# Kernel tuning notes

Measured on AMD Instinct MI355X. Metric: run time of the kernel, lower is better.

The kernel has to match this reference:

```python
import jax, jax.numpy as jnp
import numpy as np

BETA = 0.001
VAR_MIN = 1e-7


def setup_inputs() -> dict:
    key = jax.random.key(0)
    ks = jax.random.split(key, 16)
    B, IN, N, Z, S = 2048, 32, 1024, 8, 8
    f32 = jnp.float32
    return {
        "batch": jax.random.normal(ks[0], (B, IN, N, 2), f32),
        "labels": jax.random.randint(ks[1], (B, 1), 0, 2).astype(jnp.int32),
        "eps1": jax.random.normal(ks[2], (B, S, Z), f32),
        "eps2": jax.random.normal(ks[3], (B, S, Z), f32),
        "W1": jax.random.normal(ks[4], (IN, 32), f32) / np.sqrt(IN),
        "b1": jax.random.normal(ks[5], (32,), f32) * 0.01,
        "W2": jax.random.normal(ks[6], (32, 32), f32) / np.sqrt(32),
        "b2": jax.random.normal(ks[7], (32,), f32) * 0.01,
        "Wmu": jax.random.normal(ks[8], (32, Z), f32) / np.sqrt(32),
        "bmu": jax.random.normal(ks[9], (Z,), f32) * 0.01,
        "Wv": jax.random.normal(ks[10], (32, Z), f32) / np.sqrt(32),
        "bv": jax.random.normal(ks[11], (Z,), f32) * 0.01,
        "sw": jax.random.normal(ks[12], (1, 1), f32),
        "sb": jax.random.normal(ks[13], (1,), f32),
    }


def _cal_z(data, W1, b1, W2, b2, Wmu, bmu, Wv, bv):
    # data: [B, IN, N] -> points [B, N, IN]
    x = jnp.transpose(data, (0, 2, 1))
    h = jax.nn.relu(x @ W1 + b1)
    h = jax.nn.relu(h @ W2 + b2)
    mu = h @ Wmu + bmu                    # [B, N, Z]
    var = jax.nn.softplus(h @ Wv + bv)    # [B, N, Z]
    var = jnp.maximum(var, VAR_MIN)
    var_pog = 1.0 / jnp.sum(1.0 / var, axis=1)  # [B, Z]
    # Faithful to torch source: var is reassigned before mu update, so
    # mu = var_pog * sum(mu / var_pog) == sum(mu) over the N axis.
    mu_pog = jnp.sum(mu, axis=1)                # [B, Z]
    return mu_pog, var_pog


def _kl(mu, var):
    # KL(N(mu, sqrt(var)) || N(0, 1)), elementwise, then mean
    return jnp.mean(-0.5 * jnp.log(var) + 0.5 * (var + mu * mu) - 0.5)


def reference(batch, labels, eps1, eps2, W1, b1, W2, b2, Wmu, bmu, Wv, bv, sw, sb):
    mu1, var1 = _cal_z(batch[:, :, :, 0], W1, b1, W2, b2, Wmu, bmu, Wv, bv)
    mu2, var2 = _cal_z(batch[:, :, :, 1], W1, b1, W2, b2, Wmu, bmu, Wv, bv)

    kl = (_kl(mu1, var1) + _kl(mu2, var2)) * BETA

    # rsample: mu + sigma * eps, [B, S, Z]
    z1 = mu1[:, None, :] + jnp.sqrt(var1)[:, None, :] * eps1
    z2 = mu2[:, None, :] + jnp.sqrt(var2)[:, None, :] * eps2

    # pairwise distances over the S x S sample grid: [B, S, S]
    diff = z1[:, :, None, :] - z2[:, None, :, :]
    dist = jnp.sqrt(jnp.sum(diff * diff, axis=-1))

    a = jax.nn.softplus(sw[0, 0])
    p = jax.nn.sigmoid(-a * dist + sb[0])
    loss1 = -jnp.log(p)
    loss_1 = jnp.mean(loss1, axis=(1, 2), keepdims=False)[:, None]  # [B, 1]
    # Faithful bug in torch source: loss0 is never assigned, stays zero,
    # so the (1 - labels) term contributes nothing.
    labels_f = labels.astype(loss_1.dtype)
    soft = jnp.mean(loss_1 * labels_f)

    return kl + soft
```

## Files before the change

### kernel.cpp

```cpp
#include <hip/hip_runtime.h>
#include <hip/hip_bf16.h>

#define B_   2048
#define N_   1024
#define BETA 0.001f
#define VAR_MIN 1e-7f

#define PTS   64
#define NSTG  (N_ / PTS)
#define RF    128

typedef __attribute__((ext_vector_type(8))) short  bf16x8;
typedef __attribute__((ext_vector_type(4))) float  f32x4;
typedef __attribute__((ext_vector_type(4))) unsigned int u32x4;

__device__ __forceinline__ unsigned short f2bf_u(float x) {
    __hip_bfloat16 h = __float2bfloat16(x);
    return __builtin_bit_cast(unsigned short, h);
}
__device__ __forceinline__ unsigned int cvtpk(float lo, float hi) {
    unsigned int r;
    asm("v_cvt_pk_bf16_f32 %0, %1, %2" : "=v"(r) : "v"(lo), "v"(hi));
    return r;
}
__device__ __forceinline__ float softplus_cheap(float x) {
    float sp = __logf(1.f + __expf(x));
    return x > 15.f ? x : sp;
}
__device__ __forceinline__ float rcp_fast(float x) {
    return __builtin_amdgcn_rcpf(x);
}
__device__ __forceinline__ float softplus_ref(float x) {
    return x > 20.f ? x : log1pf(expf(x));
}
__device__ __forceinline__ float iv_of(float x) {
    return rcp_fast(fmaxf(softplus_cheap(x), VAR_MIN));
}

__device__ __forceinline__ int kperm(int k) {
    return 4 * (k >> 3) + (k & 3) + 16 * ((k >> 2) & 1);
}

extern "C" __global__ void hib_prep(const float* __restrict__ W1,
                                    const float* __restrict__ W2,
                                    const float* __restrict__ Wmu,
                                    const float* __restrict__ Wv,
                                    unsigned short* __restrict__ wf)
{
    const int l = threadIdx.x;
    const int r = l & 15, kb = l >> 4;
    const int kbr = r >> 2, ri = r & 3;
#pragma unroll
    for (int j = 0; j < 8; j++) {
        const int k1 = kb * 8 + j;
        const int kp = kperm(k1);
        wf[(0 * 64 + l) * 8 + j] = f2bf_u(W1[k1 * 32 + r]);
        wf[(1 * 64 + l) * 8 + j] = f2bf_u(W1[k1 * 32 + 16 + r]);
        wf[(2 * 64 + l) * 8 + j] = f2bf_u(W2[kp * 32 + r]);
        wf[(3 * 64 + l) * 8 + j] = f2bf_u(W2[kp * 32 + 16 + r]);
        wf[(4 * 64 + l) * 8 + j] = f2bf_u(ri < 2 ? Wmu[kp * 8 + 2 * kbr + ri]
                                                 : Wv[kp * 8 + 2 * kbr + (ri - 2)]);
    }
}

__device__ __forceinline__ bf16x8 pack_relu(f32x4 a, f32x4 b) {
    u32x4 w;
    w[0] = cvtpk(fmaxf(a[0], 0.f), fmaxf(a[1], 0.f));
    w[1] = cvtpk(fmaxf(a[2], 0.f), fmaxf(a[3], 0.f));
    w[2] = cvtpk(fmaxf(b[0], 0.f), fmaxf(b[1], 0.f));
    w[3] = cvtpk(fmaxf(b[2], 0.f), fmaxf(b[3], 0.f));
    return __builtin_bit_cast(bf16x8, w);
}

__device__ __forceinline__ void red16(f32x4& v) {
#pragma unroll
    for (int off = 8; off; off >>= 1) {
        v[0] += __shfl_down(v[0], off);
        v[1] += __shfl_down(v[1], off);
        v[2] += __shfl_down(v[2], off);
        v[3] += __shfl_down(v[3], off);
    }
}

__device__ __forceinline__ void stage_issue(const float* __restrict__ bbase,
                                            float* __restrict__ ldsbuf,
                                            int st, int wid, int l)
{
    const int sub = l >> 5, lo = l & 31;
#pragma unroll
    for (int q = 0; q < 4; ++q) {
        const int row = wid * 8 + q * 2;
        const float* gs = bbase + (size_t)(row + sub) * (2 * N_) + st * RF + lo * 4;
        __builtin_amdgcn_global_load_lds(
            (const __attribute__((address_space(1))) unsigned int*)gs,
            (__attribute__((address_space(3))) unsigned int*)&ldsbuf[row * RF],
            16, 0, 0);
    }
}

__global__ void __launch_bounds__(256, 4)
hib_mfma(const float* __restrict__ batch,
         const int* __restrict__ labels,
         const float* __restrict__ eps1, const float* __restrict__ eps2,
         const unsigned short* __restrict__ wf,
         const float* __restrict__ b1, const float* __restrict__ b2,
         const float* __restrict__ bmu, const float* __restrict__ bv,
         const float* __restrict__ sw, const float* __restrict__ sb,
         float* __restrict__ out)
{
    __shared__ float lds[2][32 * RF];
    __shared__ float sacc[32];

    const int tid = threadIdx.x;
    const int b   = blockIdx.x;
    const int wid = tid >> 6, l = tid & 63;
    const int c   = l & 15, kb = l >> 4;

    if (tid < 32) sacc[tid] = 0.f;

    const bf16x8* wfv = (const bf16x8*)wf;
    const bf16x8 A1a = wfv[0 * 64 + l], A1b = wfv[1 * 64 + l];
    const bf16x8 A2a = wfv[2 * 64 + l], A2b = wfv[3 * 64 + l];
    const bf16x8 Ahd = wfv[4 * 64 + l];

    const int r4 = 4 * kb;
    const int z2 = 2 * kb;
    f32x4 c1a, c1b, c2a, c2b, chd;
    c1a[0] = b1[r4];      c1a[1] = b1[r4 + 1];      c1a[2] = b1[r4 + 2];      c1a[3] = b1[r4 + 3];
    c1b[0] = b1[16 + r4]; c1b[1] = b1[16 + r4 + 1]; c1b[2] = b1[16 + r4 + 2]; c1b[3] = b1[16 + r4 + 3];
    c2a[0] = b2[r4];      c2a[1] = b2[r4 + 1];      c2a[2] = b2[r4 + 2];      c2a[3] = b2[r4 + 3];
    c2b[0] = b2[16 + r4]; c2b[1] = b2[16 + r4 + 1]; c2b[2] = b2[16 + r4 + 2]; c2b[3] = b2[16 + r4 + 3];
    chd[0] = bmu[z2]; chd[1] = bmu[z2 + 1];
    chd[2] = bv[z2];  chd[3] = bv[z2 + 1];

    f32x4 acc0 = {0.f, 0.f, 0.f, 0.f};
    f32x4 acc1 = {0.f, 0.f, 0.f, 0.f};

    const float* bbase = batch + (size_t)b * 32 * (2 * N_);

    stage_issue(bbase, lds[0], 0, wid, l);
    __syncthreads();

    int buf = 0;
#pragma unroll 1
    for (int t = 0; t < NSTG; ++t) {
        if (t + 1 < NSTG)
            stage_issue(bbase, lds[buf ^ 1], t + 1, wid, l);

        float2 xr[8];
#pragma unroll
        for (int j = 0; j < 8; j++)
            xr[j] = *(const float2*)&lds[buf][(kb * 8 + j) * RF + (wid * 16 + c) * 2];

        u32x4 w0, w1;
        w0[0] = cvtpk(xr[0].x, xr[1].x); w0[1] = cvtpk(xr[2].x, xr[3].x);
        w0[2] = cvtpk(xr[4].x, xr[5].x); w0[3] = cvtpk(xr[6].x, xr[7].x);
        w1[0] = cvtpk(xr[0].y, xr[1].y); w1[1] = cvtpk(xr[2].y, xr[3].y);
        w1[2] = cvtpk(xr[4].y, xr[5].y); w1[3] = cvtpk(xr[6].y, xr[7].y);
        const bf16x8 f0 = __builtin_bit_cast(bf16x8, w0);
        const bf16x8 f1 = __builtin_bit_cast(bf16x8, w1);

        f32x4 d1a0 = __builtin_amdgcn_mfma_f32_16x16x32_bf16(A1a, f0, c1a, 0, 0, 0);
        f32x4 d1b0 = __builtin_amdgcn_mfma_f32_16x16x32_bf16(A1b, f0, c1b, 0, 0, 0);
        f32x4 d1a1 = __builtin_amdgcn_mfma_f32_16x16x32_bf16(A1a, f1, c1a, 0, 0, 0);
        f32x4 d1b1 = __builtin_amdgcn_mfma_f32_16x16x32_bf16(A1b, f1, c1b, 0, 0, 0);

        bf16x8 p20 = pack_relu(d1a0, d1b0);
        bf16x8 p21 = pack_relu(d1a1, d1b1);

        f32x4 d2a0 = __builtin_amdgcn_mfma_f32_16x16x32_bf16(A2a, p20, c2a, 0, 0, 0);
        f32x4 d2b0 = __builtin_amdgcn_mfma_f32_16x16x32_bf16(A2b, p20, c2b, 0, 0, 0);
        f32x4 d2a1 = __builtin_amdgcn_mfma_f32_16x16x32_bf16(A2a, p21, c2a, 0, 0, 0);
        f32x4 d2b1 = __builtin_amdgcn_mfma_f32_16x16x32_bf16(A2b, p21, c2b, 0, 0, 0);

        bf16x8 p30 = pack_relu(d2a0, d2b0);
        bf16x8 p31 = pack_relu(d2a1, d2b1);

        f32x4 e0 = __builtin_amdgcn_mfma_f32_16x16x32_bf16(Ahd, p30, chd, 0, 0, 0);
        f32x4 e1 = __builtin_amdgcn_mfma_f32_16x16x32_bf16(Ahd, p31, chd, 0, 0, 0);

        acc0[0] += e0[0];        acc0[1] += e0[1];
        acc0[2] += iv_of(e0[2]); acc0[3] += iv_of(e0[3]);
        acc1[0] += e1[0];        acc1[1] += e1[1];
        acc1[2] += iv_of(e1[2]); acc1[3] += iv_of(e1[3]);

        __syncthreads();
        buf ^= 1;
    }

    red16(acc0);
    red16(acc1);

    if (c == 0) {
        atomicAdd(&sacc[z2],          acc0[0]);
        atomicAdd(&sacc[z2 + 1],      acc0[1]);
        atomicAdd(&sacc[16 + z2],     acc0[2]);
        atomicAdd(&sacc[16 + z2 + 1], acc0[3]);
        atomicAdd(&sacc[8 + z2],      acc1[0]);
        atomicAdd(&sacc[8 + z2 + 1],  acc1[1]);
        atomicAdd(&sacc[24 + z2],     acc1[2]);
        atomicAdd(&sacc[24 + z2 + 1], acc1[3]);
    }
    __syncthreads();

    if (tid < 64) {
        const float a    = softplus_ref(sw[0]);
        const float sbv_ = sb[0];

        float muA[8], muB[8], sgA[8], sgB[8];
#pragma unroll
        for (int z = 0; z < 8; z++) {
            muA[z] = sacc[z];
            muB[z] = sacc[8 + z];
            sgA[z] = sqrtf(1.0f / sacc[16 + z]);
            sgB[z] = sqrtf(1.0f / sacc[24 + z]);
        }
        const int i = tid >> 3, j = tid & 7;
        float d2 = 0.f;
#pragma unroll
        for (int z = 0; z < 8; z++) {
            float e1 = eps1[((size_t)b * 8 + i) * 8 + z];
            float e2 = eps2[((size_t)b * 8 + j) * 8 + z];
            float zz1 = fmaf(sgA[z], e1, muA[z]);
            float zz2 = fmaf(sgB[z], e2, muB[z]);
            float d = zz1 - zz2;
            d2 = fmaf(d, d, d2);
        }
        const float lab = (float)labels[b];
        float contrib = softplus_ref(a * sqrtf(d2) - sbv_) * lab
                      * (1.0f / (64.0f * (float)B_));

        if (tid < 16) {
            const int cc = tid >> 3, z = tid & 7;
            float iv  = sacc[16 + cc * 8 + z];
            float var = 1.0f / iv;
            float m   = sacc[cc * 8 + z];
            contrib += (-0.5f * logf(var) + 0.5f * (var + m * m) - 0.5f)
                       * (BETA / (8.0f * (float)B_));
        }
#pragma unroll
        for (int off = 32; off; off >>= 1) contrib += __shfl_down(contrib, off);
        if (tid == 0) atomicAdd(out, contrib);
    }
}

extern "C" void kernel_launch(void* const* d_in, const int* in_sizes, int n_in,
                              void* d_out, int out_size, void* d_ws, size_t ws_size,
                              hipStream_t stream)
{
    (void)in_sizes; (void)n_in; (void)out_size; (void)ws_size;
    const float* batch  = (const float*)d_in[0];
    const int*   labels = (const int*)  d_in[1];
    const float* eps1   = (const float*)d_in[2];
    const float* eps2   = (const float*)d_in[3];
    const float* W1     = (const float*)d_in[4];
    const float* b1     = (const float*)d_in[5];
    const float* W2     = (const float*)d_in[6];
    const float* b2     = (const float*)d_in[7];
    const float* Wmu    = (const float*)d_in[8];
    const float* bmu    = (const float*)d_in[9];
    const float* Wv     = (const float*)d_in[10];
    const float* bv     = (const float*)d_in[11];
    const float* sw     = (const float*)d_in[12];
    const float* sb     = (const float*)d_in[13];

    unsigned short* wf = (unsigned short*)d_ws;

    hipMemsetAsync(d_out, 0, sizeof(float), stream);
    hib_prep<<<1, 64, 0, stream>>>(W1, W2, Wmu, Wv, wf);
    hib_mfma<<<B_, 256, 0, stream>>>(batch, labels, eps1, eps2, wf,
                                     b1, b2, bmu, bv, sw, sb, (float*)d_out);
}
```

Before: 128.1 us.

## Give each wave a private double-buffered LDS slice and drop block barriers

```diff
diff --git a/kernel.cpp b/kernel.cpp
--- a/kernel.cpp
+++ b/kernel.cpp
@@ -6,9 +6,7 @@
 #define BETA 0.001f
 #define VAR_MIN 1e-7f
 
-#define PTS   64
-#define NSTG  (N_ / PTS)
-#define RF    128
+#define NIT  16
 
 typedef __attribute__((ext_vector_type(8))) short  bf16x8;
 typedef __attribute__((ext_vector_type(4))) float  f32x4;
@@ -82,18 +80,19 @@
     }
 }
 
-__device__ __forceinline__ void stage_issue(const float* __restrict__ bbase,
-                                            float* __restrict__ ldsbuf,
-                                            int st, int wid, int l)
-{
-    const int sub = l >> 5, lo = l & 31;
+__device__ __forceinline__ void stage_wp(const float* __restrict__ bbase,
+                                         float* __restrict__ buf,
+                                         int it, int wid, int l)
+{
+    const int lrow = l >> 3, lcol = (l & 7) * 4;
+    const int colbase = (wid * 256 + it * 16) * 2;
 #pragma unroll
     for (int q = 0; q < 4; ++q) {
-        const int row = wid * 8 + q * 2;
-        const float* gs = bbase + (size_t)(row + sub) * (2 * N_) + st * RF + lo * 4;
+        const int row = q * 8 + lrow;
+        const float* gs = bbase + (size_t)row * (2 * N_) + colbase + lcol;
         __builtin_amdgcn_global_load_lds(
             (const __attribute__((address_space(1))) unsigned int*)gs,
-            (__attribute__((address_space(3))) unsigned int*)&ldsbuf[row * RF],
+            (__attribute__((address_space(3))) unsigned int*)&buf[q * 8 * 32],
             16, 0, 0);
     }
 }
@@ -108,7 +107,7 @@
          const float* __restrict__ sw, const float* __restrict__ sb,
          float* __restrict__ out)
 {
-    __shared__ float lds[2][32 * RF];
+    __shared__ float lds[4][2][32 * 32];
     __shared__ float sacc[32];
 
     const int tid = threadIdx.x;
@@ -137,20 +136,21 @@
     f32x4 acc1 = {0.f, 0.f, 0.f, 0.f};
 
     const float* bbase = batch + (size_t)b * 32 * (2 * N_);
-
-    stage_issue(bbase, lds[0], 0, wid, l);
+    float* bufA = &lds[wid][0][0];
+    float* bufB = &lds[wid][1][0];
+
+    stage_wp(bbase, bufA, 0, wid, l);
+    stage_wp(bbase, bufB, 1, wid, l);
     __syncthreads();
 
-    int buf = 0;
 #pragma unroll 1
-    for (int t = 0; t < NSTG; ++t) {
-        if (t + 1 < NSTG)
-            stage_issue(bbase, lds[buf ^ 1], t + 1, wid, l);
+    for (int it = 0; it < NIT; ++it) {
+        float* cur = (it & 1) ? bufB : bufA;
 
         float2 xr[8];
 #pragma unroll
         for (int j = 0; j < 8; j++)
-            xr[j] = *(const float2*)&lds[buf][(kb * 8 + j) * RF + (wid * 16 + c) * 2];
+            xr[j] = *(const float2*)&cur[(kb * 8 + j) * 32 + c * 2];
 
         u32x4 w0, w1;
         w0[0] = cvtpk(xr[0].x, xr[1].x); w0[1] = cvtpk(xr[2].x, xr[3].x);
@@ -160,6 +160,12 @@
         const bf16x8 f0 = __builtin_bit_cast(bf16x8, w0);
         const bf16x8 f1 = __builtin_bit_cast(bf16x8, w1);
 
+        asm volatile("s_waitcnt lgkmcnt(0)" ::: "memory");
+        __builtin_amdgcn_sched_barrier(0);
+        if (it + 2 < NIT)
+            stage_wp(bbase, cur, it + 2, wid, l);
+        __builtin_amdgcn_sched_barrier(0);
+
         f32x4 d1a0 = __builtin_amdgcn_mfma_f32_16x16x32_bf16(A1a, f0, c1a, 0, 0, 0);
         f32x4 d1b0 = __builtin_amdgcn_mfma_f32_16x16x32_bf16(A1b, f0, c1b, 0, 0, 0);
         f32x4 d1a1 = __builtin_amdgcn_mfma_f32_16x16x32_bf16(A1a, f1, c1a, 0, 0, 0);
@@ -184,8 +190,11 @@
         acc1[0] += e1[0];        acc1[1] += e1[1];
         acc1[2] += iv_of(e1[2]); acc1[3] += iv_of(e1[3]);
 
-        __syncthreads();
-        buf ^= 1;
+        if (it < NIT - 2)
+            asm volatile("s_waitcnt vmcnt(4)" ::: "memory");
+        else if (it == NIT - 2)
+            asm volatile("s_waitcnt vmcnt(0)" ::: "memory");
+        __builtin_amdgcn_sched_barrier(0);
     }
 
     red16(acc0);
```

New measurement: 112.8 us, median of 2. 12.0% less time.
